# Performance work log

Measured on AMD Instinct MI355X. Metric: run time of the kernel, lower is better.

The kernel has to match this reference:

```python
import jax, jax.numpy as jnp
import numpy as np

N_NODES = 10000
N_EDGES = 320000
IN_DIM = 256
DIM = 256
HID = 256
OUT_DIM = 64
LAYERS = 4
NEG_SLOPE = 0.2


def setup_inputs() -> dict:
    key = jax.random.key(0)
    ks = jax.random.split(key, 12)
    s = 0.05
    return {
        "x": jax.random.normal(ks[0], (N_NODES, IN_DIM), jnp.float32),
        "edge_index": jax.random.randint(ks[1], (2, N_EDGES), 0, N_NODES, jnp.int64),
        "lin1_w": jax.random.normal(ks[2], (IN_DIM, DIM), jnp.float32) * s,
        "lin1_b": jnp.zeros((DIM,), jnp.float32),
        "gat_w": jax.random.normal(ks[3], (LAYERS, DIM, DIM), jnp.float32) * s,
        "gat_asrc": jax.random.normal(ks[4], (LAYERS, DIM), jnp.float32) * s,
        "gat_adst": jax.random.normal(ks[5], (LAYERS, DIM), jnp.float32) * s,
        "gat_b": jnp.zeros((LAYERS, DIM), jnp.float32),
        "lstm_wih": jax.random.normal(ks[6], (LAYERS, 4 * HID, 2 * DIM), jnp.float32) * s,
        "lstm_whh": jax.random.normal(ks[7], (LAYERS, 4 * HID, HID), jnp.float32) * s,
        "lin2_w": jax.random.normal(ks[8], (DIM, OUT_DIM), jnp.float32) * s,
        "lin2_b": jnp.zeros((OUT_DIM,), jnp.float32),
    }


def _gat_layer(x, src, dst, n, W, a_src, a_dst, b):
    # PyG GATConv (heads=1, concat=True): project, edge attention, scatter-softmax over dst
    xw = x @ W                                   # [N, D]
    a_s = xw @ a_src                             # [N]
    a_d = xw @ a_dst                             # [N]
    alpha = a_s[src] + a_d[dst]                  # [E]
    alpha = jnp.where(alpha > 0, alpha, NEG_SLOPE * alpha)  # leaky_relu
    m = jax.ops.segment_max(alpha, dst, num_segments=n)
    e = jnp.exp(alpha - m[dst])
    denom = jax.ops.segment_sum(e, dst, num_segments=n)
    coef = e / denom[dst]                        # softmax over edges sharing dst
    out = jax.ops.segment_sum(coef[:, None] * xw[src], dst, num_segments=n)
    return out + b


def reference(x, edge_index, lin1_w, lin1_b, gat_w, gat_asrc, gat_adst, gat_b,
              lstm_wih, lstm_whh, lin2_w, lin2_b):
    n = x.shape[0]
    # add self loops (GATConv default)
    loops = jnp.arange(n, dtype=edge_index.dtype)
    src = jnp.concatenate([edge_index[0], loops])
    dst = jnp.concatenate([edge_index[1], loops])

    x0 = x @ lin1_w + lin1_b                     # [N, DIM]
    h_tmps = [jnp.tanh(_gat_layer(x0, src, dst, n, gat_w[i], gat_asrc[i], gat_adst[i], gat_b[i]))
              for i in range(LAYERS)]

    h = jnp.zeros((n, HID), x0.dtype)
    c = jnp.zeros((n, HID), x0.dtype)
    xc = x0
    for i in range(LAYERS):
        inp = jnp.concatenate([h_tmps[i], xc], axis=-1)          # [N, 2*DIM]
        gates = inp @ lstm_wih[i].T + h @ lstm_whh[i].T          # [N, 4*HID]
        ig, fg, gg, og = jnp.split(gates, 4, axis=-1)            # torch gate order i,f,g,o
        c = jax.nn.sigmoid(fg) * c + jax.nn.sigmoid(ig) * jnp.tanh(gg)
        h = jax.nn.sigmoid(og) * jnp.tanh(c)
        xc = h
    return xc @ lin2_w + lin2_b
```

## Files before the change

### kernel.cpp

```cpp
#include <hip/hip_runtime.h>
#include <hip/hip_bf16.h>
#include <math.h>

#define N_NODES 10000
#define E_RAW   320000
#define E_TOT   330000
#define DIM     256
#define HID     256
#define OUTD    64
#define LAYERS  4

typedef short    short8 __attribute__((ext_vector_type(8)));
typedef float    f32x4  __attribute__((ext_vector_type(4)));
typedef _Float16 h4v    __attribute__((ext_vector_type(4)));

__device__ __forceinline__ ushort f2bf(float f) {
    union { float f; unsigned u; } v; v.f = f;
    unsigned r = v.u + 0x7FFF + ((v.u >> 16) & 1);
    return (ushort)(r >> 16);
}
__device__ __forceinline__ float bf2f(ushort h) {
    union { unsigned u; float f; } v; v.u = ((unsigned)h) << 16;
    return v.f;
}
__device__ __forceinline__ void split_bf(float f, ushort& hi, ushort& lo) {
    hi = f2bf(f);
    lo = f2bf(f - bf2f(hi));
}

__global__ void edge_hist(const int* __restrict__ ei, int* __restrict__ deg) {
    int e = blockIdx.x * blockDim.x + threadIdx.x;
    if (e >= E_TOT) return;
    int d = (e < E_RAW) ? ei[E_RAW + e] : (e - E_RAW);
    atomicAdd(&deg[d], 1);
}

__global__ __launch_bounds__(1024) void scan_deg(const int* __restrict__ deg,
                                                 int* __restrict__ row_start) {
    __shared__ int ps[1024];
    int t = threadIdx.x;
    int begin = t * 10;
    int end   = begin + 10; if (end > N_NODES) end = N_NODES;
    int s = 0;
    for (int i = begin; i < end; ++i) s += deg[i];
    ps[t] = s;
    __syncthreads();
    for (int off = 1; off < 1024; off <<= 1) {
        int v = (t >= off) ? ps[t - off] : 0;
        __syncthreads();
        ps[t] += v;
        __syncthreads();
    }
    int excl = (t == 0) ? 0 : ps[t - 1];
    for (int i = begin; i < end; ++i) {
        row_start[i] = excl;
        excl += deg[i];
    }
    if (t == 1023) row_start[N_NODES] = ps[1023];
}

__global__ void edge_scatter(const int* __restrict__ ei, const int* __restrict__ row_start,
                             int* __restrict__ cursor, int* __restrict__ ssrc) {
    int e = blockIdx.x * blockDim.x + threadIdx.x;
    if (e >= E_TOT) return;
    int s, d;
    if (e < E_RAW) { s = ei[e]; d = ei[E_RAW + e]; }
    else           { s = e - E_RAW; d = s; }
    int pos = row_start[d] + atomicAdd(&cursor[d], 1);
    ssrc[pos] = s;
}

__global__ void split_lstm_w(const float* __restrict__ wih, const float* __restrict__ whh,
                             ushort* __restrict__ wh, ushort* __restrict__ wl) {
    int gid = blockIdx.x * blockDim.x + threadIdx.x;
    if (gid >= LAYERS * 1024 * 512 / 4) return;
    int i4  = gid * 4;
    int l   = i4 / (1024 * 512);
    int rem = i4 - l * (1024 * 512);
    int R   = rem / 512;
    int k   = rem - R * 512;
    float4 v = *reinterpret_cast<const float4*>(wih + ((size_t)(l * 1024 + R) * 512) + k);
    if (l > 0 && k >= 256) {
        float4 w2 = *reinterpret_cast<const float4*>(whh + ((size_t)(l * 1024 + R) * 256) + (k - 256));
        v.x += w2.x; v.y += w2.y; v.z += w2.z; v.w += w2.w;
    }
    int gate = R >> 8, hu = R & 255;
    int gp = ((hu >> 4) << 6) + (gate << 4) + (hu & 15);
    ushort4 h4, l4;
    split_bf(v.x, h4.x, l4.x); split_bf(v.y, h4.y, l4.y);
    split_bf(v.z, h4.z, l4.z); split_bf(v.w, h4.w, l4.w);
    size_t dst = (size_t)(l * 1024 + gp) * 512 + k;
    *reinterpret_cast<ushort4*>(wh + dst) = h4;
    *reinterpret_cast<ushort4*>(wl + dst) = l4;
}

__global__ void split_gat_w(const float* __restrict__ gat_w,
                            ushort* __restrict__ gh, ushort* __restrict__ gl) {
    int gid = blockIdx.x * blockDim.x + threadIdx.x;
    if (gid >= LAYERS * 256 * 64) return;
    int l   = gid >> 14;
    int rem = gid & 16383;
    int n   = rem >> 6;
    int k4  = (rem & 63) * 4;
    ushort4 h4, l4;
    float v0 = gat_w[((size_t)l * 256 + k4 + 0) * 256 + n];
    float v1 = gat_w[((size_t)l * 256 + k4 + 1) * 256 + n];
    float v2 = gat_w[((size_t)l * 256 + k4 + 2) * 256 + n];
    float v3 = gat_w[((size_t)l * 256 + k4 + 3) * 256 + n];
    split_bf(v0, h4.x, l4.x); split_bf(v1, h4.y, l4.y);
    split_bf(v2, h4.z, l4.z); split_bf(v3, h4.w, l4.w);
    size_t dst = ((size_t)l * 256 + n) * 256 + k4;
    *reinterpret_cast<ushort4*>(gh + dst) = h4;
    *reinterpret_cast<ushort4*>(gl + dst) = l4;
}

__global__ void split_wT(const float* __restrict__ w, ushort* __restrict__ oh,
                         ushort* __restrict__ ol, int K, int N) {
    int gid = blockIdx.x * blockDim.x + threadIdx.x;
    if (gid >= N * K) return;
    int n = gid / K, k = gid - n * K;
    ushort hi, lo;
    split_bf(w[(size_t)k * N + n], hi, lo);
    oh[gid] = hi; ol[gid] = lo;
}

__global__ void split_x(const float* __restrict__ x, ushort* __restrict__ xh,
                        ushort* __restrict__ xl, int total4) {
    int gid = blockIdx.x * blockDim.x + threadIdx.x;
    if (gid >= total4) return;
    float4 v = *reinterpret_cast<const float4*>(x + (size_t)gid * 4);
    ushort4 h4, l4;
    split_bf(v.x, h4.x, l4.x); split_bf(v.y, h4.y, l4.y);
    split_bf(v.z, h4.z, l4.z); split_bf(v.w, h4.w, l4.w);
    *reinterpret_cast<ushort4*>(xh + (size_t)gid * 4) = h4;
    *reinterpret_cast<ushort4*>(xl + (size_t)gid * 4) = l4;
}

__global__ __launch_bounds__(256, 2) void gemm_bf3(
        const ushort* __restrict__ Ah0, const ushort* __restrict__ Al0,
        const ushort* __restrict__ Ah1, const ushort* __restrict__ Al1,
        const ushort* __restrict__ Bh,  const ushort* __restrict__ Bl,
        const float* __restrict__ bias,
        float* __restrict__ C, ushort* __restrict__ Oh, ushort* __restrict__ Ol,
        _Float16* __restrict__ Xh, float* __restrict__ Cc,
        int M, int N, int K, int mode) {
    __shared__ ushort Ahs[128][40];
    __shared__ ushort Als[128][40];
    __shared__ ushort Bhs[128][40];
    __shared__ ushort Bls[128][40];

    int tid  = threadIdx.x;
    int lane = tid & 63;
    int w    = tid >> 6;
    int wm   = w >> 1, wn = w & 1;
    int bm = blockIdx.x * 128, bn = blockIdx.y * 128;

    f32x4 acc[4][4];
#pragma unroll
    for (int i = 0; i < 4; ++i)
#pragma unroll
        for (int j = 0; j < 4; ++j)
#pragma unroll
            for (int q = 0; q < 4; ++q) acc[i][j][q] = 0.f;

    int r  = tid >> 1;
    int kh = (tid & 1) * 16;
    bool aok = (bm + r) < M;
    bool bok = (bn + r) < N;

    int l15 = lane & 15;
    int kg  = (lane >> 4) * 8;

    for (int k0 = 0; k0 < K; k0 += 32) {
        const ushort* ah = (k0 < 256) ? Ah0 : Ah1;
        const ushort* al = (k0 < 256) ? Al0 : Al1;
        int ka = (k0 & 255) + kh;
        size_t aoff = (size_t)(bm + r) * 256 + ka;
        size_t boff = (size_t)(bn + r) * K + k0 + kh;

        uint4 ah0v = {0,0,0,0}, ah1v = {0,0,0,0}, al0v = {0,0,0,0}, al1v = {0,0,0,0};
        uint4 bh0v = {0,0,0,0}, bh1v = {0,0,0,0}, bl0v = {0,0,0,0}, bl1v = {0,0,0,0};
        if (aok) {
            ah0v = *reinterpret_cast<const uint4*>(ah + aoff);
            ah1v = *reinterpret_cast<const uint4*>(ah + aoff + 8);
            al0v = *reinterpret_cast<const uint4*>(al + aoff);
            al1v = *reinterpret_cast<const uint4*>(al + aoff + 8);
        }
        if (bok) {
            bh0v = *reinterpret_cast<const uint4*>(Bh + boff);
            bh1v = *reinterpret_cast<const uint4*>(Bh + boff + 8);
            bl0v = *reinterpret_cast<const uint4*>(Bl + boff);
            bl1v = *reinterpret_cast<const uint4*>(Bl + boff + 8);
        }

        __syncthreads();
        *reinterpret_cast<uint4*>(&Ahs[r][kh])     = ah0v;
        *reinterpret_cast<uint4*>(&Ahs[r][kh + 8]) = ah1v;
        *reinterpret_cast<uint4*>(&Als[r][kh])     = al0v;
        *reinterpret_cast<uint4*>(&Als[r][kh + 8]) = al1v;
        *reinterpret_cast<uint4*>(&Bhs[r][kh])     = bh0v;
        *reinterpret_cast<uint4*>(&Bhs[r][kh + 8]) = bh1v;
        *reinterpret_cast<uint4*>(&Bls[r][kh])     = bl0v;
        *reinterpret_cast<uint4*>(&Bls[r][kh + 8]) = bl1v;
        __syncthreads();

        short8 afh[4], afl[4], bfh[4], bfl[4];
#pragma unroll
        for (int i = 0; i < 4; ++i) {
            int ar = wm * 64 + i * 16 + l15;
            afh[i] = *reinterpret_cast<const short8*>(&Ahs[ar][kg]);
            afl[i] = *reinterpret_cast<const short8*>(&Als[ar][kg]);
        }
#pragma unroll
        for (int j = 0; j < 4; ++j) {
            int br = wn * 64 + j * 16 + l15;
            bfh[j] = *reinterpret_cast<const short8*>(&Bhs[br][kg]);
            bfl[j] = *reinterpret_cast<const short8*>(&Bls[br][kg]);
        }
#pragma unroll
        for (int i = 0; i < 4; ++i)
#pragma unroll
            for (int j = 0; j < 4; ++j)
                acc[i][j] = __builtin_amdgcn_mfma_f32_16x16x32_bf16(afh[i], bfh[j], acc[i][j], 0, 0, 0);
#pragma unroll
        for (int i = 0; i < 4; ++i)
#pragma unroll
            for (int j = 0; j < 4; ++j)
                acc[i][j] = __builtin_amdgcn_mfma_f32_16x16x32_bf16(afh[i], bfl[j], acc[i][j], 0, 0, 0);
#pragma unroll
        for (int i = 0; i < 4; ++i)
#pragma unroll
            for (int j = 0; j < 4; ++j)
                acc[i][j] = __builtin_amdgcn_mfma_f32_16x16x32_bf16(afl[i], bfh[j], acc[i][j], 0, 0, 0);
    }

    if (mode == 3) {
        int hu = (((bn + wn * 64) >> 6) << 4) + l15;
#pragma unroll
        for (int i = 0; i < 4; ++i) {
#pragma unroll
            for (int rr = 0; rr < 4; ++rr) {
                int n = bm + wm * 64 + i * 16 + (lane >> 4) * 4 + rr;
                if (n >= M) continue;
                float ig = acc[i][0][rr], fg = acc[i][1][rr];
                float gg = acc[i][2][rr], og = acc[i][3][rr];
                float si = 1.f / (1.f + expf(-ig));
                float sf = 1.f / (1.f + expf(-fg));
                float so = 1.f / (1.f + expf(-og));
                size_t o = (size_t)n * 256 + hu;
                float cn = sf * Cc[o] + si * tanhf(gg);
                float hn = so * tanhf(cn);
                Cc[o] = cn;
                ushort hi2, lo2; split_bf(hn, hi2, lo2);
                Oh[o] = hi2; Ol[o] = lo2;
            }
        }
        return;
    }
#pragma unroll
    for (int i = 0; i < 4; ++i) {
        int row0 = bm + wm * 64 + i * 16 + (lane >> 4) * 4;
#pragma unroll
        for (int j = 0; j < 4; ++j) {
            int col = bn + wn * 64 + j * 16 + l15;
            if (col >= N) continue;
            float bs = bias ? bias[col] : 0.f;
#pragma unroll
            for (int rr = 0; rr < 4; ++rr) {
                int row = row0 + rr;
                if (row >= M) continue;
                float o = acc[i][j][rr] + bs;
                if (mode == 0) {
                    C[(size_t)row * N + col] = o;
                } else if (mode == 1) {
                    Xh[((size_t)(col >> 8) * M + row) * 256 + (col & 255)] = (_Float16)o;
                } else {
                    ushort hi, lo; split_bf(o, hi, lo);
                    Oh[(size_t)row * N + col] = hi;
                    Ol[(size_t)row * N + col] = lo;
                }
            }
        }
    }
}

__global__ void compute_asd(const _Float16* __restrict__ xw_all,
                            const float* __restrict__ asrc_all,
                            const float* __restrict__ adst_all,
                            float* __restrict__ a_s, float* __restrict__ a_d) {
    int gt = blockIdx.x * blockDim.x + threadIdx.x;
    int gw = gt >> 6, lane = gt & 63;
    if (gw >= LAYERS * N_NODES) return;
    int l = gw / N_NODES;
    h4v v = *reinterpret_cast<const h4v*>(xw_all + (size_t)gw * 256 + lane * 4);
    float4 sa = *reinterpret_cast<const float4*>(asrc_all + l * 256 + lane * 4);
    float4 da = *reinterpret_cast<const float4*>(adst_all + l * 256 + lane * 4);
    float v0 = (float)v[0], v1 = (float)v[1], v2 = (float)v[2], v3 = (float)v[3];
    float s = v0*sa.x + v1*sa.y + v2*sa.z + v3*sa.w;
    float d = v0*da.x + v1*da.y + v2*da.z + v3*da.w;
    for (int off = 32; off; off >>= 1) {
        s += __shfl_down(s, off);
        d += __shfl_down(d, off);
    }
    if (lane == 0) { a_s[gw] = s; a_d[gw] = d; }
}

__global__ __launch_bounds__(256) void gat_aggregate(const _Float16* __restrict__ xw_all,
                                                     const float* __restrict__ a_s,
                                                     const float* __restrict__ a_d,
                                                     const int* __restrict__ row_start,
                                                     const int* __restrict__ ssrc,
                                                     const float* __restrict__ gat_b,
                                                     ushort* __restrict__ htmph,
                                                     ushort* __restrict__ htmpl) {
    int gw = blockIdx.x * 4 + (threadIdx.x >> 6);
    if (gw >= LAYERS * N_NODES) return;
    int l = gw / N_NODES, n = gw - l * N_NODES;
    int lane = threadIdx.x & 63;
    int beg = row_start[n], end = row_start[n + 1];
    const _Float16* xw = xw_all + (size_t)l * N_NODES * 256;
    const float* asl = a_s + (size_t)l * N_NODES;
    float adn = a_d[gw];

    float lm = -3.4e38f;
    for (int e = beg + lane; e < end; e += 64) {
        float s = asl[ssrc[e]] + adn;
        s = (s > 0.f) ? s : 0.2f * s;
        lm = fmaxf(lm, s);
    }
    for (int off = 32; off; off >>= 1) lm = fmaxf(lm, __shfl_xor(lm, off));
    float m = lm;

    float ls = 0.f;
    for (int e = beg + lane; e < end; e += 64) {
        float s = asl[ssrc[e]] + adn;
        s = (s > 0.f) ? s : 0.2f * s;
        ls += expf(s - m);
    }
    for (int off = 32; off; off >>= 1) ls += __shfl_xor(ls, off);
    float inv = 1.f / ls;

    float4 acc = make_float4(0.f, 0.f, 0.f, 0.f);
    for (int ch = beg; ch < end; ch += 64) {
        int e = ch + lane;
        float cfo = 0.f; int s0o = 0;
        if (e < end) {
            s0o = ssrc[e];
            float s = asl[s0o] + adn;
            s = (s > 0.f) ? s : 0.2f * s;
            cfo = expf(s - m) * inv;
        }
        int len = end - ch; if (len > 64) len = 64;
        for (int j = 0; j < len; ++j) {
            float cf = __shfl(cfo, j);
            int   s0 = __shfl(s0o, j);
            h4v v = *reinterpret_cast<const h4v*>(xw + (size_t)s0 * 256 + lane * 4);
            acc.x += cf * (float)v[0]; acc.y += cf * (float)v[1];
            acc.z += cf * (float)v[2]; acc.w += cf * (float)v[3];
        }
    }
    float4 b = *reinterpret_cast<const float4*>(gat_b + l * 256 + lane * 4);
    ushort4 h4, l4;
    split_bf(tanhf(acc.x + b.x), h4.x, l4.x);
    split_bf(tanhf(acc.y + b.y), h4.y, l4.y);
    split_bf(tanhf(acc.z + b.z), h4.z, l4.z);
    split_bf(tanhf(acc.w + b.w), h4.w, l4.w);
    size_t dst = (size_t)gw * 256 + lane * 4;
    *reinterpret_cast<ushort4*>(htmph + dst) = h4;
    *reinterpret_cast<ushort4*>(htmpl + dst) = l4;
}

extern "C" void kernel_launch(void* const* d_in, const int* in_sizes, int n_in,
                              void* d_out, int out_size, void* d_ws, size_t ws_size,
                              hipStream_t stream) {
    const float* x        = (const float*)d_in[0];
    const int*   ei       = (const int*)  d_in[1];
    const float* lin1_w   = (const float*)d_in[2];
    const float* lin1_b   = (const float*)d_in[3];
    const float* gat_w    = (const float*)d_in[4];
    const float* gat_asrc = (const float*)d_in[5];
    const float* gat_adst = (const float*)d_in[6];
    const float* gat_b    = (const float*)d_in[7];
    const float* lstm_wih = (const float*)d_in[8];
    const float* lstm_whh = (const float*)d_in[9];
    const float* lin2_w   = (const float*)d_in[10];
    const float* lin2_b   = (const float*)d_in[11];
    float* out = (float*)d_out;

    size_t off = 0;
    auto alloc = [&](size_t bytes) -> void* {
        void* p = (char*)d_ws + off;
        off = (off + bytes + 255) & ~(size_t)255;
        return p;
    };
    ushort* xh     = (ushort*)alloc((size_t)N_NODES * DIM * 2);
    ushort* xl     = (ushort*)alloc((size_t)N_NODES * DIM * 2);
    ushort* x0h    = (ushort*)alloc((size_t)N_NODES * DIM * 2);
    ushort* x0l    = (ushort*)alloc((size_t)N_NODES * DIM * 2);
    _Float16* xwh  = (_Float16*)alloc((size_t)LAYERS * N_NODES * DIM * 2);
    ushort* htmph  = (ushort*)alloc((size_t)LAYERS * N_NODES * DIM * 2);
    ushort* htmpl  = (ushort*)alloc((size_t)LAYERS * N_NODES * DIM * 2);
    float*  c      = (float*) alloc((size_t)N_NODES * HID * 4);
    ushort* hbh[2], *hbl[2];
    hbh[0] = (ushort*)alloc((size_t)N_NODES * HID * 2);
    hbl[0] = (ushort*)alloc((size_t)N_NODES * HID * 2);
    hbh[1] = (ushort*)alloc((size_t)N_NODES * HID * 2);
    hbl[1] = (ushort*)alloc((size_t)N_NODES * HID * 2);
    float*  a_s    = (float*) alloc((size_t)LAYERS * N_NODES * 4);
    float*  a_d    = (float*) alloc((size_t)LAYERS * N_NODES * 4);
    int* row_start = (int*)   alloc((size_t)(N_NODES + 1) * 4);
    int* cursor    = (int*)   alloc((size_t)N_NODES * 4);
    int* ssrc      = (int*)   alloc((size_t)E_TOT * 4);
    ushort* wlh    = (ushort*)alloc((size_t)LAYERS * 1024 * 512 * 2);
    ushort* wll    = (ushort*)alloc((size_t)LAYERS * 1024 * 512 * 2);
    ushort* gwh    = (ushort*)alloc((size_t)LAYERS * 256 * 256 * 2);
    ushort* gwl    = (ushort*)alloc((size_t)LAYERS * 256 * 256 * 2);
    ushort* l1h    = (ushort*)alloc((size_t)256 * 256 * 2);
    ushort* l1l    = (ushort*)alloc((size_t)256 * 256 * 2);
    ushort* l2h    = (ushort*)alloc((size_t)64 * 256 * 2);
    ushort* l2l    = (ushort*)alloc((size_t)64 * 256 * 2);

    hipMemsetAsync(cursor, 0, N_NODES * 4, stream);
    edge_hist<<<(E_TOT + 255) / 256, 256, 0, stream>>>(ei, cursor);
    scan_deg<<<1, 1024, 0, stream>>>(cursor, row_start);
    hipMemsetAsync(cursor, 0, N_NODES * 4, stream);
    edge_scatter<<<(E_TOT + 255) / 256, 256, 0, stream>>>(ei, row_start, cursor, ssrc);

    split_x<<<(N_NODES * DIM / 4 + 255) / 256, 256, 0, stream>>>(x, xh, xl, N_NODES * DIM / 4);
    split_lstm_w<<<(LAYERS * 1024 * 512 / 4 + 255) / 256, 256, 0, stream>>>(lstm_wih, lstm_whh, wlh, wll);
    split_gat_w<<<(LAYERS * 256 * 64 + 255) / 256, 256, 0, stream>>>(gat_w, gwh, gwl);
    split_wT<<<(256 * 256 + 255) / 256, 256, 0, stream>>>(lin1_w, l1h, l1l, 256, 256);
    split_wT<<<(64 * 256 + 255) / 256, 256, 0, stream>>>(lin2_w, l2h, l2l, 256, 64);

    hipMemsetAsync(c, 0, (size_t)N_NODES * HID * 4, stream);

    {
        dim3 grid((N_NODES + 127) / 128, 256 / 128);
        gemm_bf3<<<grid, 256, 0, stream>>>(xh, xl, xh, xl,
                                           l1h, l1l, lin1_b,
                                           nullptr, x0h, x0l, nullptr, nullptr,
                                           N_NODES, 256, 256, 2);
    }

    {
        dim3 grid((N_NODES + 127) / 128, (LAYERS * DIM) / 128);
        gemm_bf3<<<grid, 256, 0, stream>>>(x0h, x0l, x0h, x0l,
                                           gwh, gwl, nullptr,
                                           nullptr, nullptr, nullptr, xwh, nullptr,
                                           N_NODES, LAYERS * DIM, 256, 1);
        int waves = LAYERS * N_NODES;
        compute_asd<<<(waves * 64 + 255) / 256, 256, 0, stream>>>(xwh, gat_asrc, gat_adst,
                                                                  a_s, a_d);
        gat_aggregate<<<(waves + 3) / 4, 256, 0, stream>>>(xwh, a_s, a_d, row_start, ssrc,
                                                           gat_b, htmph, htmpl);
    }

    for (int l = 0; l < LAYERS; ++l) {
        const ushort* xch = (l == 0) ? x0h : hbh[(l - 1) & 1];
        const ushort* xcl = (l == 0) ? x0l : hbl[(l - 1) & 1];
        dim3 gridL((N_NODES + 127) / 128, 1024 / 128);
        gemm_bf3<<<gridL, 256, 0, stream>>>(
            htmph + (size_t)l * N_NODES * DIM, htmpl + (size_t)l * N_NODES * DIM,
            xch, xcl,
            wlh + (size_t)l * 1024 * 512, wll + (size_t)l * 1024 * 512,
            nullptr, nullptr, hbh[l & 1], hbl[l & 1], nullptr, c,
            N_NODES, 1024, 512, 3);
    }

    {
        dim3 grid((N_NODES + 127) / 128, 1);
        gemm_bf3<<<grid, 256, 0, stream>>>(hbh[1], hbl[1], hbh[1], hbl[1],
                                           l2h, l2l, lin2_b,
                                           out, nullptr, nullptr, nullptr, nullptr,
                                           N_NODES, OUTD, 256, 0);
    }
}
```

Measured before the change: 553.6 us.

## Stage GEMM tiles via direct global-to-LDS loads and remap workgroups across XCDs

The bf16x3 GEMM now loads A/B hi/lo tiles straight from global memory into LDS using global_load_lds, with each wave owning one operand and writing a fragment-ordered layout that MFMA reads without padding. This removes the register round trip and the explicit LDS stores. Workgroup indices are also remapped so neighbouring tiles land on the same XCD for better L2 reuse. Bounds checks on rows were removed, so the code over-allocates lin2 buffers and pads the arena to tolerate out-of-range reads, which risks reading garbage rows past M.

```diff
diff --git a/kernel.cpp b/kernel.cpp
--- a/kernel.cpp
+++ b/kernel.cpp
@@ -26,6 +26,13 @@
 __device__ __forceinline__ void split_bf(float f, ushort& hi, ushort& lo) {
     hi = f2bf(f);
     lo = f2bf(f - bf2f(hi));
+}
+
+__device__ __forceinline__ void gload16(const void* g, void* l) {
+    __builtin_amdgcn_global_load_lds(
+        (const __attribute__((address_space(1))) unsigned int*)g,
+        (__attribute__((address_space(3))) unsigned int*)l,
+        16, 0, 0);
 }
 
 __global__ void edge_hist(const int* __restrict__ ei, int* __restrict__ deg) {
@@ -144,16 +151,20 @@
         float* __restrict__ C, ushort* __restrict__ Oh, ushort* __restrict__ Ol,
         _Float16* __restrict__ Xh, float* __restrict__ Cc,
         int M, int N, int K, int mode) {
-    __shared__ ushort Ahs[128][40];
-    __shared__ ushort Als[128][40];
-    __shared__ ushort Bhs[128][40];
-    __shared__ ushort Bls[128][40];
+    __shared__ ushort lds[16384];
 
     int tid  = threadIdx.x;
     int lane = tid & 63;
     int w    = tid >> 6;
     int wm   = w >> 1, wn = w & 1;
-    int bm = blockIdx.x * 128, bn = blockIdx.y * 128;
+
+    int gx = gridDim.x;
+    int nwg = gx * gridDim.y;
+    int orig = blockIdx.y * gx + blockIdx.x;
+    int q8 = nwg >> 3, r7 = nwg & 7;
+    int xcd = orig & 7, rest = orig >> 3;
+    int wg = (xcd < r7 ? xcd * (q8 + 1) : r7 * (q8 + 1) + (xcd - r7) * q8) + rest;
+    int bm = (wg % gx) * 128, bn = (wg / gx) * 128;
 
     f32x4 acc[4][4];
 #pragma unroll
@@ -161,61 +172,35 @@
 #pragma unroll
         for (int j = 0; j < 4; ++j)
 #pragma unroll
-            for (int q = 0; q < 4; ++q) acc[i][j][q] = 0.f;
-
-    int r  = tid >> 1;
-    int kh = (tid & 1) * 16;
-    bool aok = (bm + r) < M;
-    bool bok = (bn + r) < N;
+            for (int qq = 0; qq < 4; ++qq) acc[i][j][qq] = 0.f;
 
     int l15 = lane & 15;
-    int kg  = (lane >> 4) * 8;
+    int skg = (lane >> 4) * 8;
 
     for (int k0 = 0; k0 < K; k0 += 32) {
-        const ushort* ah = (k0 < 256) ? Ah0 : Ah1;
-        const ushort* al = (k0 < 256) ? Al0 : Al1;
-        int ka = (k0 & 255) + kh;
-        size_t aoff = (size_t)(bm + r) * 256 + ka;
-        size_t boff = (size_t)(bn + r) * K + k0 + kh;
-
-        uint4 ah0v = {0,0,0,0}, ah1v = {0,0,0,0}, al0v = {0,0,0,0}, al1v = {0,0,0,0};
-        uint4 bh0v = {0,0,0,0}, bh1v = {0,0,0,0}, bl0v = {0,0,0,0}, bl1v = {0,0,0,0};
-        if (aok) {
-            ah0v = *reinterpret_cast<const uint4*>(ah + aoff);
-            ah1v = *reinterpret_cast<const uint4*>(ah + aoff + 8);
-            al0v = *reinterpret_cast<const uint4*>(al + aoff);
-            al1v = *reinterpret_cast<const uint4*>(al + aoff + 8);
-        }
-        if (bok) {
-            bh0v = *reinterpret_cast<const uint4*>(Bh + boff);
-            bh1v = *reinterpret_cast<const uint4*>(Bh + boff + 8);
-            bl0v = *reinterpret_cast<const uint4*>(Bl + boff);
-            bl1v = *reinterpret_cast<const uint4*>(Bl + boff + 8);
-        }
-
+        const ushort* gs;
+        if (w == 0)      gs = (k0 < 256) ? Ah0 : Ah1;
+        else if (w == 1) gs = (k0 < 256) ? Al0 : Al1;
+        else if (w == 2) gs = Bh;
+        else             gs = Bl;
+        int    rowbase = (w < 2) ? bm : bn;
+        size_t rstride = (w < 2) ? 256 : (size_t)K;
+        int    kk      = (w < 2) ? ((k0 & 255) + skg) : (k0 + skg);
+#pragma unroll
+        for (int blk = 0; blk < 8; ++blk) {
+            const ushort* g = gs + (size_t)(rowbase + blk * 16 + l15) * rstride + kk;
+            int lidx = __builtin_amdgcn_readfirstlane(w * 4096 + blk * 512);
+            gload16(g, (void*)&lds[lidx]);
+        }
         __syncthreads();
-        *reinterpret_cast<uint4*>(&Ahs[r][kh])     = ah0v;
-        *reinterpret_cast<uint4*>(&Ahs[r][kh + 8]) = ah1v;
-        *reinterpret_cast<uint4*>(&Als[r][kh])     = al0v;
-        *reinterpret_cast<uint4*>(&Als[r][kh + 8]) = al1v;
-        *reinterpret_cast<uint4*>(&Bhs[r][kh])     = bh0v;
-        *reinterpret_cast<uint4*>(&Bhs[r][kh + 8]) = bh1v;
-        *reinterpret_cast<uint4*>(&Bls[r][kh])     = bl0v;
-        *reinterpret_cast<uint4*>(&Bls[r][kh + 8]) = bl1v;
-        __syncthreads();
 
         short8 afh[4], afl[4], bfh[4], bfl[4];
 #pragma unroll
         for (int i = 0; i < 4; ++i) {
-            int ar = wm * 64 + i * 16 + l15;
-            afh[i] = *reinterpret_cast<const short8*>(&Ahs[ar][kg]);
-            afl[i] = *reinterpret_cast<const short8*>(&Als[ar][kg]);
-        }
-#pragma unroll
-        for (int j = 0; j < 4; ++j) {
-            int br = wn * 64 + j * 16 + l15;
-            bfh[j] = *reinterpret_cast<const short8*>(&Bhs[br][kg]);
-            bfl[j] = *reinterpret_cast<const short8*>(&Bls[br][kg]);
+            afh[i] = *reinterpret_cast<const short8*>(&lds[        (wm * 4 + i) * 512 + lane * 8]);
+            afl[i] = *reinterpret_cast<const short8*>(&lds[ 4096 + (wm * 4 + i) * 512 + lane * 8]);
+            bfh[i] = *reinterpret_cast<const short8*>(&lds[ 8192 + (wn * 4 + i) * 512 + lane * 8]);
+            bfl[i] = *reinterpret_cast<const short8*>(&lds[12288 + (wn * 4 + i) * 512 + lane * 8]);
         }
 #pragma unroll
         for (int i = 0; i < 4; ++i)
@@ -232,6 +217,7 @@
 #pragma unroll
             for (int j = 0; j < 4; ++j)
                 acc[i][j] = __builtin_amdgcn_mfma_f32_16x16x32_bf16(afl[i], bfh[j], acc[i][j], 0, 0, 0);
+        __syncthreads();
     }
 
     if (mode == 3) {
@@ -417,8 +403,9 @@
     ushort* gwl    = (ushort*)alloc((size_t)LAYERS * 256 * 256 * 2);
     ushort* l1h    = (ushort*)alloc((size_t)256 * 256 * 2);
     ushort* l1l    = (ushort*)alloc((size_t)256 * 256 * 2);
-    ushort* l2h    = (ushort*)alloc((size_t)64 * 256 * 2);
-    ushort* l2l    = (ushort*)alloc((size_t)64 * 256 * 2);
+    ushort* l2h    = (ushort*)alloc((size_t)128 * 256 * 2);
+    ushort* l2l    = (ushort*)alloc((size_t)128 * 256 * 2);
+    (void)alloc(65536);
 
     hipMemsetAsync(cursor, 0, N_NODES * 4, stream);
     edge_hist<<<(E_TOT + 255) / 256, 256, 0, stream>>>(ei, cursor);
```

Measured after the change: 595.8 us. 1.08x slower.
